# Kernel optimization log

Hardware: AMD Instinct MI355X
Metric: run time of the kernel (lower is better)

The kernel has to match this reference:

```python
import jax, jax.numpy as jnp
import numpy as np


def setup_inputs() -> dict:
    key = jax.random.key(0)
    k1, k2, k3, k4 = jax.random.split(key, 4)
    B, C = 32768, 1000
    y_pred = jax.random.normal(k1, (B, C), dtype=jnp.float32)
    y_true = jax.random.randint(k2, (B,), 0, C, dtype=jnp.int64)
    distance_matrix = jax.random.uniform(k3, (C, C), dtype=jnp.float32)
    fix_layer = jax.random.normal(k4, (C, C), dtype=jnp.float32)
    return {"y_pred": y_pred, "y_true": y_true,
            "distance_matrix": distance_matrix, "fix_layer": fix_layer}


def reference(y_pred, y_true, distance_matrix, fix_layer):
    # log_softmax over classes
    logp = jax.nn.log_softmax(y_pred, axis=1)              # [B, C]
    pred = jnp.argmax(y_pred, axis=1)                      # [B]
    # h_matrix[i] = distance_matrix[pred_i, target_i] / max(distance_matrix)
    h = distance_matrix[pred, y_true] / jnp.max(distance_matrix)  # [B]
    # loss = -sum(log_softmax * one_hot(target) * h) / B
    # one_hot gather == logp[i, target_i]
    per_sample = logp[jnp.arange(y_pred.shape[0]), y_true] * h    # [B]
    # NOTE: fix_layer feeds h_weights in the original, which is dead code.
    loss = -jnp.sum(per_sample) / y_true.shape[0]
    return loss
```

## Files before the change

### kernel.cpp

```cpp
#include <hip/hip_runtime.h>
#include <math.h>

#define NCLASS 1000
#define NCHUNK 250
#define ROWS_PER_WAVE 4
#define WAVES_PER_BLOCK 4
#define ROWS_PER_BLOCK (ROWS_PER_WAVE * WAVES_PER_BLOCK)

__global__ __launch_bounds__(256) void hce_main(
    const float* __restrict__ y_pred,
    const int*   __restrict__ y_true,
    const float* __restrict__ D,
    float* __restrict__ partial,
    int nb, int dsize)
{
    const int tid  = threadIdx.x;
    const int lane = tid & 63;
    const int wave = tid >> 6;
    const int b    = blockIdx.x;

    float dm = -1.0f;
    for (int i = b * 256 + tid; i < dsize; i += nb * 256)
        dm = fmaxf(dm, D[i]);
    #pragma unroll
    for (int off = 32; off; off >>= 1)
        dm = fmaxf(dm, __shfl_xor(dm, off, 64));

    __shared__ float smax[WAVES_PER_BLOCK];
    __shared__ float ssum[WAVES_PER_BLOCK];
    if (lane == 0) smax[wave] = dm;

    float acc = 0.0f;
    const int row0 = b * ROWS_PER_BLOCK + wave * ROWS_PER_WAVE;
    for (int r = 0; r < ROWS_PER_WAVE; ++r) {
        const int row = row0 + r;
        const float4* rp4 = (const float4*)(y_pred + (size_t)row * NCLASS);

        float4 v[4];
        #pragma unroll
        for (int t = 0; t < 4; ++t) {
            int c = lane + 64 * t;
            if (c < NCHUNK) v[t] = rp4[c];
        }
        const int nt = (lane + 192 < NCHUNK) ? 4 : 3;

        float m = -INFINITY; int arg = 0;
        #pragma unroll
        for (int t = 0; t < 4; ++t) {
            if (t < nt) {
                int col = 4 * (lane + 64 * t);
                if (v[t].x > m) { m = v[t].x; arg = col;     }
                if (v[t].y > m) { m = v[t].y; arg = col + 1; }
                if (v[t].z > m) { m = v[t].z; arg = col + 2; }
                if (v[t].w > m) { m = v[t].w; arg = col + 3; }
            }
        }
        #pragma unroll
        for (int off = 32; off; off >>= 1) {
            float om = __shfl_xor(m,   off, 64);
            int   oa = __shfl_xor(arg, off, 64);
            if (om > m || (om == m && oa < arg)) { m = om; arg = oa; }
        }

        float s = 0.0f;
        #pragma unroll
        for (int t = 0; t < 4; ++t) {
            if (t < nt) {
                s += __expf(v[t].x - m) + __expf(v[t].y - m)
                   + __expf(v[t].z - m) + __expf(v[t].w - m);
            }
        }
        #pragma unroll
        for (int off = 32; off; off >>= 1)
            s += __shfl_xor(s, off, 64);

        if (lane == 0) {
            int   tgt  = y_true[row];
            float xt   = y_pred[(size_t)row * NCLASS + tgt];
            float logp = xt - m - __logf(s);
            float d    = D[arg * NCLASS + tgt];
            acc += logp * d;
        }
    }

    if (lane == 0) ssum[wave] = acc;
    __syncthreads();
    if (tid == 0) {
        partial[b]      = ssum[0] + ssum[1] + ssum[2] + ssum[3];
        partial[nb + b] = fmaxf(fmaxf(smax[0], smax[1]),
                                fmaxf(smax[2], smax[3]));
    }
}

__global__ __launch_bounds__(256) void hce_finalize(
    const float* __restrict__ partial, int nb,
    float* __restrict__ out, float invB)
{
    const int tid  = threadIdx.x;
    const int lane = tid & 63;
    const int wave = tid >> 6;
    float s = 0.0f, mx = -1.0f;
    for (int i = tid; i < nb; i += 256) {
        s  += partial[i];
        mx  = fmaxf(mx, partial[nb + i]);
    }
    #pragma unroll
    for (int off = 32; off; off >>= 1) {
        s  += __shfl_xor(s, off, 64);
        mx  = fmaxf(mx, __shfl_xor(mx, off, 64));
    }
    __shared__ float ss[4], sm[4];
    if (lane == 0) { ss[wave] = s; sm[wave] = mx; }
    __syncthreads();
    if (tid == 0) {
        float S = ss[0] + ss[1] + ss[2] + ss[3];
        float M = fmaxf(fmaxf(sm[0], sm[1]), fmaxf(sm[2], sm[3]));
        out[0] = -S * invB / M;
    }
}

extern "C" void kernel_launch(void* const* d_in, const int* in_sizes, int n_in,
                              void* d_out, int out_size, void* d_ws, size_t ws_size,
                              hipStream_t stream) {
    const float* y_pred = (const float*)d_in[0];
    const int*   y_true = (const int*)  d_in[1];
    const float* D      = (const float*)d_in[2];
    float* out = (float*)d_out;
    float* ws  = (float*)d_ws;

    const int B     = in_sizes[1];
    const int dsize = in_sizes[2];
    const int nb    = B / ROWS_PER_BLOCK;

    hce_main<<<nb, 256, 0, stream>>>(y_pred, y_true, D, ws, nb, dsize);
    hce_finalize<<<1, 256, 0, stream>>>(ws, nb, out, 1.0f / (float)B);
}
```

Measured before the change: 197.9 us.

## Fuse finalize into main kernel via last-block atomic counter and batch row loads

Merges the finalize kernel into the main kernel: each block publishes its partial sum and max, bumps an atomic counter, and the last block to arrive does the final reduction. This removes the second kernel launch but adds a memset launch for the counter. It also issues loads for all four rows per wave up front so more memory requests are in flight, which raises register pressure.

```diff
diff --git a/kernel.cpp b/kernel.cpp
--- a/kernel.cpp
+++ b/kernel.cpp
@@ -3,16 +3,18 @@
 
 #define NCLASS 1000
 #define NCHUNK 250
-#define ROWS_PER_WAVE 4
-#define WAVES_PER_BLOCK 4
-#define ROWS_PER_BLOCK (ROWS_PER_WAVE * WAVES_PER_BLOCK)
+#define RPW 4
+#define WPB 4
+#define RPB (RPW * WPB)
 
-__global__ __launch_bounds__(256) void hce_main(
+__global__ __launch_bounds__(256) void hce_fused(
     const float* __restrict__ y_pred,
     const int*   __restrict__ y_true,
     const float* __restrict__ D,
     float* __restrict__ partial,
-    int nb, int dsize)
+    unsigned int* __restrict__ counter,
+    float* __restrict__ out,
+    int nb, int dsize, float invB)
 {
     const int tid  = threadIdx.x;
     const int lane = tid & 63;
@@ -22,37 +24,32 @@
     float dm = -1.0f;
     for (int i = b * 256 + tid; i < dsize; i += nb * 256)
         dm = fmaxf(dm, D[i]);
+
+    const int row0 = b * RPB + wave * RPW;
+    float4 v[RPW][4];
     #pragma unroll
-    for (int off = 32; off; off >>= 1)
-        dm = fmaxf(dm, __shfl_xor(dm, off, 64));
-
-    __shared__ float smax[WAVES_PER_BLOCK];
-    __shared__ float ssum[WAVES_PER_BLOCK];
-    if (lane == 0) smax[wave] = dm;
-
-    float acc = 0.0f;
-    const int row0 = b * ROWS_PER_BLOCK + wave * ROWS_PER_WAVE;
-    for (int r = 0; r < ROWS_PER_WAVE; ++r) {
-        const int row = row0 + r;
-        const float4* rp4 = (const float4*)(y_pred + (size_t)row * NCLASS);
-
-        float4 v[4];
+    for (int r = 0; r < RPW; ++r) {
+        const float4* rp4 = (const float4*)(y_pred + (size_t)(row0 + r) * NCLASS);
         #pragma unroll
         for (int t = 0; t < 4; ++t) {
             int c = lane + 64 * t;
-            if (c < NCHUNK) v[t] = rp4[c];
+            if (c < NCHUNK) v[r][t] = rp4[c];
         }
-        const int nt = (lane + 192 < NCHUNK) ? 4 : 3;
+    }
+    const int nt = (lane < NCHUNK - 192) ? 4 : 3;
 
+    float acc = 0.0f;
+    #pragma unroll
+    for (int r = 0; r < RPW; ++r) {
         float m = -INFINITY; int arg = 0;
         #pragma unroll
         for (int t = 0; t < 4; ++t) {
             if (t < nt) {
                 int col = 4 * (lane + 64 * t);
-                if (v[t].x > m) { m = v[t].x; arg = col;     }
-                if (v[t].y > m) { m = v[t].y; arg = col + 1; }
-                if (v[t].z > m) { m = v[t].z; arg = col + 2; }
-                if (v[t].w > m) { m = v[t].w; arg = col + 3; }
+                if (v[r][t].x > m) { m = v[r][t].x; arg = col;     }
+                if (v[r][t].y > m) { m = v[r][t].y; arg = col + 1; }
+                if (v[r][t].z > m) { m = v[r][t].z; arg = col + 2; }
+                if (v[r][t].w > m) { m = v[r][t].w; arg = col + 3; }
             }
         }
         #pragma unroll
@@ -66,8 +63,8 @@
         #pragma unroll
         for (int t = 0; t < 4; ++t) {
             if (t < nt) {
-                s += __expf(v[t].x - m) + __expf(v[t].y - m)
-                   + __expf(v[t].z - m) + __expf(v[t].w - m);
+                s += __expf(v[r][t].x - m) + __expf(v[r][t].y - m)
+                   + __expf(v[r][t].z - m) + __expf(v[r][t].w - m);
             }
         }
         #pragma unroll
@@ -75,47 +72,51 @@
             s += __shfl_xor(s, off, 64);
 
         if (lane == 0) {
-            int   tgt  = y_true[row];
-            float xt   = y_pred[(size_t)row * NCLASS + tgt];
-            float logp = xt - m - __logf(s);
-            float d    = D[arg * NCLASS + tgt];
-            acc += logp * d;
+            int   tgt = y_true[row0 + r];
+            float xt  = y_pred[(size_t)(row0 + r) * NCLASS + tgt];
+            acc += (xt - m - __logf(s)) * D[arg * NCLASS + tgt];
         }
     }
 
-    if (lane == 0) ssum[wave] = acc;
+    #pragma unroll
+    for (int off = 32; off; off >>= 1)
+        dm = fmaxf(dm, __shfl_xor(dm, off, 64));
+
+    __shared__ float ssum[WPB], smax[WPB];
+    __shared__ int lastflag;
+    if (lane == 0) { ssum[wave] = acc; smax[wave] = dm; }
     __syncthreads();
+
     if (tid == 0) {
-        partial[b]      = ssum[0] + ssum[1] + ssum[2] + ssum[3];
-        partial[nb + b] = fmaxf(fmaxf(smax[0], smax[1]),
-                                fmaxf(smax[2], smax[3]));
+        float bs = ssum[0] + ssum[1] + ssum[2] + ssum[3];
+        float bm = fmaxf(fmaxf(smax[0], smax[1]), fmaxf(smax[2], smax[3]));
+        __hip_atomic_store(&partial[b],      bs, __ATOMIC_RELAXED, __HIP_MEMORY_SCOPE_AGENT);
+        __hip_atomic_store(&partial[nb + b], bm, __ATOMIC_RELAXED, __HIP_MEMORY_SCOPE_AGENT);
+        unsigned prev = __hip_atomic_fetch_add(counter, 1u,
+                            __ATOMIC_ACQ_REL, __HIP_MEMORY_SCOPE_AGENT);
+        lastflag = (prev == (unsigned)(nb - 1));
     }
-}
+    __syncthreads();
 
-__global__ __launch_bounds__(256) void hce_finalize(
-    const float* __restrict__ partial, int nb,
-    float* __restrict__ out, float invB)
-{
-    const int tid  = threadIdx.x;
-    const int lane = tid & 63;
-    const int wave = tid >> 6;
-    float s = 0.0f, mx = -1.0f;
-    for (int i = tid; i < nb; i += 256) {
-        s  += partial[i];
-        mx  = fmaxf(mx, partial[nb + i]);
-    }
-    #pragma unroll
-    for (int off = 32; off; off >>= 1) {
-        s  += __shfl_xor(s, off, 64);
-        mx  = fmaxf(mx, __shfl_xor(mx, off, 64));
-    }
-    __shared__ float ss[4], sm[4];
-    if (lane == 0) { ss[wave] = s; sm[wave] = mx; }
-    __syncthreads();
-    if (tid == 0) {
-        float S = ss[0] + ss[1] + ss[2] + ss[3];
-        float M = fmaxf(fmaxf(sm[0], sm[1]), fmaxf(sm[2], sm[3]));
-        out[0] = -S * invB / M;
+    if (lastflag) {
+        float s = 0.0f, mx = -1.0f;
+        for (int i = tid; i < nb; i += 256) {
+            s  += __hip_atomic_load(&partial[i],      __ATOMIC_RELAXED, __HIP_MEMORY_SCOPE_AGENT);
+            mx  = fmaxf(mx, __hip_atomic_load(&partial[nb + i],
+                                              __ATOMIC_RELAXED, __HIP_MEMORY_SCOPE_AGENT));
+        }
+        #pragma unroll
+        for (int off = 32; off; off >>= 1) {
+            s  = s + __shfl_xor(s, off, 64);
+            mx = fmaxf(mx, __shfl_xor(mx, off, 64));
+        }
+        if (lane == 0) { ssum[wave] = s; smax[wave] = mx; }
+        __syncthreads();
+        if (tid == 0) {
+            float S = ssum[0] + ssum[1] + ssum[2] + ssum[3];
+            float M = fmaxf(fmaxf(smax[0], smax[1]), fmaxf(smax[2], smax[3]));
+            out[0] = -S * invB / M;
+        }
     }
 }
 
@@ -130,8 +131,10 @@
 
     const int B     = in_sizes[1];
     const int dsize = in_sizes[2];
-    const int nb    = B / ROWS_PER_BLOCK;
+    const int nb    = B / RPB;
 
-    hce_main<<<nb, 256, 0, stream>>>(y_pred, y_true, D, ws, nb, dsize);
-    hce_finalize<<<1, 256, 0, stream>>>(ws, nb, out, 1.0f / (float)B);
+    unsigned int* counter = (unsigned int*)(ws + 2 * (size_t)nb);
+    hipMemsetAsync(counter, 0, sizeof(unsigned int), stream);
+    hce_fused<<<nb, 256, 0, stream>>>(y_pred, y_true, D, ws, counter, out,
+                                      nb, dsize, 1.0f / (float)B);
 }
```

After: 250.6 us. 1.27x slower.

## Process two rows per wave concurrently with online softmax merge in reductions

Applied to the files above, without the earlier changes.

Each wave now loads two rows together, with all loads issued up front, instead of looping over four rows one after another. This raises memory-level parallelism and doubles the block count. The max, argmax and exp-sum are merged in a single butterfly using an online-softmax rescale, which removes the separate max-then-sum shuffle passes. The price is extra exp calls in the shuffle merge, more registers for the two rows, and more blocks redundantly scanning D for its max.

```diff
diff --git a/kernel.cpp b/kernel.cpp
--- a/kernel.cpp
+++ b/kernel.cpp
@@ -3,9 +3,9 @@
 
 #define NCLASS 1000
 #define NCHUNK 250
-#define ROWS_PER_WAVE 4
-#define WAVES_PER_BLOCK 4
-#define ROWS_PER_BLOCK (ROWS_PER_WAVE * WAVES_PER_BLOCK)
+#define RPW 2
+#define WPB 4
+#define RPB (RPW * WPB)
 
 __global__ __launch_bounds__(256) void hce_main(
     const float* __restrict__ y_pred,
@@ -19,71 +19,87 @@
     const int wave = tid >> 6;
     const int b    = blockIdx.x;
 
-    float dm = -1.0f;
+    float dm = 0.0f;
     for (int i = b * 256 + tid; i < dsize; i += nb * 256)
         dm = fmaxf(dm, D[i]);
+
+    const int row0 = b * RPB + wave * RPW;
+
+    const int tgtA = y_true[row0];
+    const int tgtB = y_true[row0 + 1];
+    const float* rowA = y_pred + (size_t)row0 * NCLASS;
+    const float* rowB = rowA + NCLASS;
+    const float xtA = rowA[tgtA];
+    const float xtB = rowB[tgtB];
+
+    const float4* pA = (const float4*)rowA;
+    const float4* pB = (const float4*)rowB;
+    float4 vA[4], vB[4];
+    #pragma unroll
+    for (int t = 0; t < 4; ++t) {
+        int c = lane + 64 * t;
+        if (c < NCHUNK) { vA[t] = pA[c]; vB[t] = pB[c]; }
+    }
+    const int nt = (lane < NCHUNK - 192) ? 4 : 3;
+
+    float mA = -INFINITY, mB = -INFINITY;
+    int   aA = 0,         aB = 0;
+    #pragma unroll
+    for (int t = 0; t < 4; ++t) {
+        if (t < nt) {
+            int col = 4 * (lane + 64 * t);
+            const float fa[4] = { vA[t].x, vA[t].y, vA[t].z, vA[t].w };
+            const float fb[4] = { vB[t].x, vB[t].y, vB[t].z, vB[t].w };
+            #pragma unroll
+            for (int j = 0; j < 4; ++j) {
+                if (fa[j] > mA) { mA = fa[j]; aA = col + j; }
+                if (fb[j] > mB) { mB = fb[j]; aB = col + j; }
+            }
+        }
+    }
+
+    float sA = 0.0f, sB = 0.0f;
+    #pragma unroll
+    for (int t = 0; t < 4; ++t) {
+        if (t < nt) {
+            sA += __expf(vA[t].x - mA) + __expf(vA[t].y - mA)
+                + __expf(vA[t].z - mA) + __expf(vA[t].w - mA);
+            sB += __expf(vB[t].x - mB) + __expf(vB[t].y - mB)
+                + __expf(vB[t].z - mB) + __expf(vB[t].w - mB);
+        }
+    }
+
+    #pragma unroll
+    for (int off = 32; off; off >>= 1) {
+        float omA = __shfl_xor(mA, off, 64);
+        int   oaA = __shfl_xor(aA, off, 64);
+        float osA = __shfl_xor(sA, off, 64);
+        float omB = __shfl_xor(mB, off, 64);
+        int   oaB = __shfl_xor(aB, off, 64);
+        float osB = __shfl_xor(sB, off, 64);
+
+        float MA = fmaxf(mA, omA);
+        sA = sA * __expf(mA - MA) + osA * __expf(omA - MA);
+        aA = (omA > mA) ? oaA : ((omA == mA) ? min(aA, oaA) : aA);
+        mA = MA;
+
+        float MB = fmaxf(mB, omB);
+        sB = sB * __expf(mB - MB) + osB * __expf(omB - MB);
+        aB = (omB > mB) ? oaB : ((omB == mB) ? min(aB, oaB) : aB);
+        mB = MB;
+    }
+
+    float contrib = 0.0f;
+    if (lane == 0) contrib = (xtA - mA - __logf(sA)) * D[aA * NCLASS + tgtA];
+    if (lane == 1) contrib = (xtB - mB - __logf(sB)) * D[aB * NCLASS + tgtB];
+    contrib += __shfl_xor(contrib, 1, 64);
+
     #pragma unroll
     for (int off = 32; off; off >>= 1)
         dm = fmaxf(dm, __shfl_xor(dm, off, 64));
 
-    __shared__ float smax[WAVES_PER_BLOCK];
-    __shared__ float ssum[WAVES_PER_BLOCK];
-    if (lane == 0) smax[wave] = dm;
-
-    float acc = 0.0f;
-    const int row0 = b * ROWS_PER_BLOCK + wave * ROWS_PER_WAVE;
-    for (int r = 0; r < ROWS_PER_WAVE; ++r) {
-        const int row = row0 + r;
-        const float4* rp4 = (const float4*)(y_pred + (size_t)row * NCLASS);
-
-        float4 v[4];
-        #pragma unroll
-        for (int t = 0; t < 4; ++t) {
-            int c = lane + 64 * t;
-            if (c < NCHUNK) v[t] = rp4[c];
-        }
-        const int nt = (lane + 192 < NCHUNK) ? 4 : 3;
-
-        float m = -INFINITY; int arg = 0;
-        #pragma unroll
-        for (int t = 0; t < 4; ++t) {
-            if (t < nt) {
-                int col = 4 * (lane + 64 * t);
-                if (v[t].x > m) { m = v[t].x; arg = col;     }
-                if (v[t].y > m) { m = v[t].y; arg = col + 1; }
-                if (v[t].z > m) { m = v[t].z; arg = col + 2; }
-                if (v[t].w > m) { m = v[t].w; arg = col + 3; }
-            }
-        }
-        #pragma unroll
-        for (int off = 32; off; off >>= 1) {
-            float om = __shfl_xor(m,   off, 64);
-            int   oa = __shfl_xor(arg, off, 64);
-            if (om > m || (om == m && oa < arg)) { m = om; arg = oa; }
-        }
-
-        float s = 0.0f;
-        #pragma unroll
-        for (int t = 0; t < 4; ++t) {
-            if (t < nt) {
-                s += __expf(v[t].x - m) + __expf(v[t].y - m)
-                   + __expf(v[t].z - m) + __expf(v[t].w - m);
-            }
-        }
-        #pragma unroll
-        for (int off = 32; off; off >>= 1)
-            s += __shfl_xor(s, off, 64);
-
-        if (lane == 0) {
-            int   tgt  = y_true[row];
-            float xt   = y_pred[(size_t)row * NCLASS + tgt];
-            float logp = xt - m - __logf(s);
-            float d    = D[arg * NCLASS + tgt];
-            acc += logp * d;
-        }
-    }
-
-    if (lane == 0) ssum[wave] = acc;
+    __shared__ float ssum[WPB], smax[WPB];
+    if (lane == 0) { ssum[wave] = contrib; smax[wave] = dm; }
     __syncthreads();
     if (tid == 0) {
         partial[b]      = ssum[0] + ssum[1] + ssum[2] + ssum[3];
@@ -99,7 +115,7 @@
     const int tid  = threadIdx.x;
     const int lane = tid & 63;
     const int wave = tid >> 6;
-    float s = 0.0f, mx = -1.0f;
+    float s = 0.0f, mx = 0.0f;
     for (int i = tid; i < nb; i += 256) {
         s  += partial[i];
         mx  = fmaxf(mx, partial[nb + i]);
@@ -130,7 +146,7 @@
 
     const int B     = in_sizes[1];
     const int dsize = in_sizes[2];
-    const int nb    = B / ROWS_PER_BLOCK;
+    const int nb    = B / RPB;
 
     hce_main<<<nb, 256, 0, stream>>>(y_pred, y_true, D, ws, nb, dsize);
     hce_finalize<<<1, 256, 0, stream>>>(ws, nb, out, 1.0f / (float)B);
```

Measured after the change: 199.2 us. About the same (+0.7%).
